# Performance work log

Hardware: AMD Instinct MI355X
Metric: run time of the kernel (lower is better)

Reference implementation:

```python
import jax, jax.numpy as jnp
import numpy as np

E, M, K, N = 32, 1024, 512, 512

def setup_inputs() -> dict:
    key = jax.random.key(0)
    k1, k2, k3 = jax.random.split(key, 3)
    A = jax.random.normal(k1, (E, M, K), dtype=jnp.float32)
    B = jax.random.normal(k2, (E, N, K), dtype=jnp.float32)
    expert_num_tokens = jax.random.randint(k3, (E,), 0, M + 1, dtype=jnp.int32)
    return {"A": A, "B": B, "expert_num_tokens": expert_num_tokens}

def reference(A, B, expert_num_tokens):
    # Per-expert GEMM: C[e] = A[e] @ B[e].T  -> [E, M, N]
    C = jnp.einsum('emk,enk->emn', A, B)
    # Rows m >= expert_num_tokens[e] are never computed/stored by the kernel;
    # zero them in the reference output.
    row_valid = jnp.arange(A.shape[1])[None, :] < expert_num_tokens[:, None]  # [E, M]
    return jnp.where(row_valid[:, :, None], C, jnp.zeros((), C.dtype))
```

## Files before the change

### kernel.cpp

```cpp
#include <hip/hip_runtime.h>
#include <hip/hip_bf16.h>

#define NE 32
#define MM 1024
#define KK 512
#define NN 512
#define BM 128
#define BN 128
#define BK 32

typedef __attribute__((ext_vector_type(8))) short bf16x8;
typedef __attribute__((ext_vector_type(4))) float floatx4;

__device__ __forceinline__ short f2bf(float f) {
  union { __hip_bfloat16 b; short s; } u;
  u.b = __float2bfloat16(f);
  return u.s;
}

extern "C" __global__ __launch_bounds__(256, 4)
void expert_gemm(const float* __restrict__ A, const float* __restrict__ B,
                 const int* __restrict__ cnts, float* __restrict__ C)
{
  const int b   = blockIdx.x;
  const int tid = threadIdx.x;

  int e = -1, mt = 0, nt = 0;
  int acc = 0;
#pragma unroll 1
  for (int i = 0; i < NE; ++i) {
    int vt = (cnts[i] + BM - 1) >> 7;
    int c4 = vt << 2;
    if (e < 0 && b < acc + c4) { int r = b - acc; e = i; mt = r >> 2; nt = r & 3; }
    acc += c4;
  }
  if (e < 0) {
    int z = b - acc, a2 = 0;
#pragma unroll 1
    for (int i = 0; i < NE; ++i) {
      int vt = (cnts[i] + BM - 1) >> 7;
      int c = 8 - vt;
      if (e < 0 && z < a2 + c) { e = i; mt = vt + (z - a2); }
      a2 += c;
    }
    if (e < 0) return;
    float* Ce = C + ((size_t)e * MM + mt * BM) * NN;
    float4 zf = make_float4(0.f, 0.f, 0.f, 0.f);
#pragma unroll
    for (int i = 0; i < 64; ++i) {
      int fidx = i * 256 + tid;
      int r = fidx >> 7, c = (fidx & 127) << 2;
      *(float4*)(Ce + (size_t)r * NN + c) = zf;
    }
    return;
  }

  const int m0 = mt * BM, n0 = nt * BN;
  const int cnt = cnts[e];
  const float* Ae = A + ((size_t)e * MM + m0) * KK;
  const float* Be = B + ((size_t)e * NN + n0) * KK;
  float* Ce = C + ((size_t)e * MM + m0) * NN + n0;

  __shared__ __align__(16) short lA[BM * BK];
  __shared__ __align__(16) short lB[BN * BK];

  const int wave = tid >> 6, lane = tid & 63;
  const int wm = (wave >> 1) * 64, wn = (wave & 1) * 64;
  const int fr = lane & 15, kh = lane >> 4;

  const int srow = tid >> 2;
  const int su   = tid & 3;

  floatx4 acc4[4][4] = {};

  for (int kt = 0; kt < KK; kt += BK) {
    float4 a0[2], a1[2], b0[2], b1[2];
#pragma unroll
    for (int p = 0; p < 2; ++p) {
      int row = srow + (p << 6);
      int col = kt + (su << 3);
      a0[p] = *(const float4*)(Ae + (size_t)row * KK + col);
      a1[p] = *(const float4*)(Ae + (size_t)row * KK + col + 4);
      b0[p] = *(const float4*)(Be + (size_t)row * KK + col);
      b1[p] = *(const float4*)(Be + (size_t)row * KK + col + 4);
    }

    __syncthreads();
#pragma unroll
    for (int p = 0; p < 2; ++p) {
      int row = srow + (p << 6);
      int unit = (row << 2) + (su ^ (row & 3));
      bf16x8 va = { f2bf(a0[p].x), f2bf(a0[p].y), f2bf(a0[p].z), f2bf(a0[p].w),
                    f2bf(a1[p].x), f2bf(a1[p].y), f2bf(a1[p].z), f2bf(a1[p].w) };
      bf16x8 vb = { f2bf(b0[p].x), f2bf(b0[p].y), f2bf(b0[p].z), f2bf(b0[p].w),
                    f2bf(b1[p].x), f2bf(b1[p].y), f2bf(b1[p].z), f2bf(b1[p].w) };
      *(bf16x8*)(lA + (unit << 3)) = va;
      *(bf16x8*)(lB + (unit << 3)) = vb;
    }
    __syncthreads();

    bf16x8 af[4], bfv[4];
#pragma unroll
    for (int i = 0; i < 4; ++i) {
      int rA = wm + (i << 4) + fr;
      af[i]  = *(const bf16x8*)(lA + ((((rA << 2) + (kh ^ (rA & 3)))) << 3));
      int rB = wn + (i << 4) + fr;
      bfv[i] = *(const bf16x8*)(lB + ((((rB << 2) + (kh ^ (rB & 3)))) << 3));
    }
#pragma unroll
    for (int i = 0; i < 4; ++i)
#pragma unroll
      for (int j = 0; j < 4; ++j)
        acc4[i][j] = __builtin_amdgcn_mfma_f32_16x16x32_bf16(af[i], bfv[j], acc4[i][j], 0, 0, 0);
  }

  const int rb_ = (lane >> 4) * 4;
#pragma unroll
  for (int i = 0; i < 4; ++i) {
#pragma unroll
    for (int r = 0; r < 4; ++r) {
      int row = wm + i * 16 + rb_ + r;
      bool valid = (m0 + row) < cnt;
#pragma unroll
      for (int j = 0; j < 4; ++j) {
        int col = wn + j * 16 + fr;
        Ce[(size_t)row * NN + col] = valid ? acc4[i][j][r] : 0.0f;
      }
    }
  }
}

extern "C" void kernel_launch(void* const* d_in, const int* in_sizes, int n_in,
                              void* d_out, int out_size, void* d_ws, size_t ws_size,
                              hipStream_t stream) {
  const float* A    = (const float*)d_in[0];
  const float* B    = (const float*)d_in[1];
  const int*   cnts = (const int*)d_in[2];
  float*       C    = (float*)d_out;

  hipLaunchKernelGGL(expert_gemm, dim3(1024), dim3(256), 0, stream, A, B, cnts, C);
}
```

Measured before the change: 159.4 us.

## Prefetch next K tile into registers and map experts to XCDs

Global loads for the next K tile are issued right after the shared-memory stores, so they overlap with the MFMA work of the current tile instead of stalling before it. Blocks are also reassigned so that each of the 8 XCDs (blockIdx mod 8) handles a fixed set of 4 experts, aiming for L2 locality of each expert's A and B data. The prefetch raises register pressure. The per-XCD split can unbalance load when expert token counts differ.

Measured after the change: 171.3 us. 1.08x slower.

```diff
diff --git a/kernel.cpp b/kernel.cpp
--- a/kernel.cpp
+++ b/kernel.cpp
@@ -22,25 +22,28 @@
 void expert_gemm(const float* __restrict__ A, const float* __restrict__ B,
                  const int* __restrict__ cnts, float* __restrict__ C)
 {
-  const int b   = blockIdx.x;
-  const int tid = threadIdx.x;
+  const int xcd  = blockIdx.x & 7;
+  const int slot = blockIdx.x >> 3;
+  const int tid  = threadIdx.x;
 
   int e = -1, mt = 0, nt = 0;
   int acc = 0;
-#pragma unroll 1
-  for (int i = 0; i < NE; ++i) {
-    int vt = (cnts[i] + BM - 1) >> 7;
+#pragma unroll
+  for (int g = 0; g < 4; ++g) {
+    int ee = xcd + (g << 3);
+    int vt = (cnts[ee] + BM - 1) >> 7;
     int c4 = vt << 2;
-    if (e < 0 && b < acc + c4) { int r = b - acc; e = i; mt = r >> 2; nt = r & 3; }
+    if (e < 0 && slot < acc + c4) { int r = slot - acc; e = ee; mt = r >> 2; nt = r & 3; }
     acc += c4;
   }
   if (e < 0) {
-    int z = b - acc, a2 = 0;
-#pragma unroll 1
-    for (int i = 0; i < NE; ++i) {
-      int vt = (cnts[i] + BM - 1) >> 7;
+    int z = slot - acc, a2 = 0;
+#pragma unroll
+    for (int g = 0; g < 4; ++g) {
+      int ee = xcd + (g << 3);
+      int vt = (cnts[ee] + BM - 1) >> 7;
       int c = 8 - vt;
-      if (e < 0 && z < a2 + c) { e = i; mt = vt + (z - a2); }
+      if (e < 0 && z < a2 + c) { e = ee; mt = vt + (z - a2); }
       a2 += c;
     }
     if (e < 0) return;
@@ -73,31 +76,43 @@
 
   floatx4 acc4[4][4] = {};
 
+  float4 pa0[2], pa1[2], pb0[2], pb1[2];
+#pragma unroll
+  for (int p = 0; p < 2; ++p) {
+    int row = srow + (p << 6);
+    int col = su << 3;
+    pa0[p] = *(const float4*)(Ae + (size_t)row * KK + col);
+    pa1[p] = *(const float4*)(Ae + (size_t)row * KK + col + 4);
+    pb0[p] = *(const float4*)(Be + (size_t)row * KK + col);
+    pb1[p] = *(const float4*)(Be + (size_t)row * KK + col + 4);
+  }
+
   for (int kt = 0; kt < KK; kt += BK) {
-    float4 a0[2], a1[2], b0[2], b1[2];
-#pragma unroll
-    for (int p = 0; p < 2; ++p) {
-      int row = srow + (p << 6);
-      int col = kt + (su << 3);
-      a0[p] = *(const float4*)(Ae + (size_t)row * KK + col);
-      a1[p] = *(const float4*)(Ae + (size_t)row * KK + col + 4);
-      b0[p] = *(const float4*)(Be + (size_t)row * KK + col);
-      b1[p] = *(const float4*)(Be + (size_t)row * KK + col + 4);
-    }
-
     __syncthreads();
 #pragma unroll
     for (int p = 0; p < 2; ++p) {
       int row = srow + (p << 6);
       int unit = (row << 2) + (su ^ (row & 3));
-      bf16x8 va = { f2bf(a0[p].x), f2bf(a0[p].y), f2bf(a0[p].z), f2bf(a0[p].w),
-                    f2bf(a1[p].x), f2bf(a1[p].y), f2bf(a1[p].z), f2bf(a1[p].w) };
-      bf16x8 vb = { f2bf(b0[p].x), f2bf(b0[p].y), f2bf(b0[p].z), f2bf(b0[p].w),
-                    f2bf(b1[p].x), f2bf(b1[p].y), f2bf(b1[p].z), f2bf(b1[p].w) };
+      bf16x8 va = { f2bf(pa0[p].x), f2bf(pa0[p].y), f2bf(pa0[p].z), f2bf(pa0[p].w),
+                    f2bf(pa1[p].x), f2bf(pa1[p].y), f2bf(pa1[p].z), f2bf(pa1[p].w) };
+      bf16x8 vb = { f2bf(pb0[p].x), f2bf(pb0[p].y), f2bf(pb0[p].z), f2bf(pb0[p].w),
+                    f2bf(pb1[p].x), f2bf(pb1[p].y), f2bf(pb1[p].z), f2bf(pb1[p].w) };
       *(bf16x8*)(lA + (unit << 3)) = va;
       *(bf16x8*)(lB + (unit << 3)) = vb;
     }
     __syncthreads();
+
+    if (kt + BK < KK) {
+#pragma unroll
+      for (int p = 0; p < 2; ++p) {
+        int row = srow + (p << 6);
+        int col = kt + BK + (su << 3);
+        pa0[p] = *(const float4*)(Ae + (size_t)row * KK + col);
+        pa1[p] = *(const float4*)(Ae + (size_t)row * KK + col + 4);
+        pb0[p] = *(const float4*)(Be + (size_t)row * KK + col);
+        pb1[p] = *(const float4*)(Be + (size_t)row * KK + col + 4);
+      }
+    }
 
     bf16x8 af[4], bfv[4];
 #pragma unroll
```
